# Optimization experiments

Hardware: AMD Instinct MI355X
Metric: run time of the kernel (lower is better)

Reference implementation:

```python
import jax, jax.numpy as jnp
import numpy as np

B, S, HID = 2, 4096, 2048
H, KV, D = 16, 4, 128
BS_, L, G, STRIDE, WTOK = 64, 4, 4, 4, 2048
SCALE = float(D) ** -0.5
NEG = -1.0e9


def _rope_tables(seq, dim):
    inv = 1.0 / (10000.0 ** (np.arange(0, dim, 2, dtype=np.float64) / dim))
    f = np.arange(seq, dtype=np.float64)[:, None] * inv[None, :]
    emb = np.concatenate([f, f], axis=-1)
    return np.cos(emb).astype(np.float32), np.sin(emb).astype(np.float32)


def _rotate_half(x):
    x1, x2 = x[..., : x.shape[-1] // 2], x[..., x.shape[-1] // 2 :]
    return jnp.concatenate([-x2, x1], axis=-1)


def _global_idx(nb, g, stride, max_away):
    # static (trace-time) computation of strided global block indices per query block
    g_idx = np.zeros((nb, g), dtype=np.int32)
    g_valid = np.zeros((nb, g), dtype=np.float32)
    for i in range(1, nb):
        cand = np.arange(max(0, i - max_away), i)
        if stride > 1:
            cand = cand[::stride]
        if cand.size == 0:
            continue
        if cand.size > g:
            cand = cand[-g:]
        s0 = g - cand.size
        g_idx[i, s0:] = cand
        g_valid[i, s0:] = 1.0
    return jnp.asarray(g_idx), jnp.asarray(g_valid)


def setup_inputs():
    key = jax.random.key(0)
    ks = jax.random.split(key, 5)
    hidden_states = jax.random.normal(ks[0], (B, S, HID), jnp.float32)
    cos_t, sin_t = _rope_tables(S, D)
    cos = jnp.broadcast_to(jnp.asarray(cos_t)[None], (B, S, D))
    sin = jnp.broadcast_to(jnp.asarray(sin_t)[None], (B, S, D))
    attention_mask_2d = jnp.ones((B, S), jnp.float32)
    sd = HID ** -0.5
    Wq = jax.random.normal(ks[1], (HID, H * D), jnp.float32) * sd
    Wk = jax.random.normal(ks[2], (HID, KV * D), jnp.float32) * sd
    Wv = jax.random.normal(ks[3], (HID, KV * D), jnp.float32) * sd
    Wo = jax.random.normal(ks[4], (H * D, HID), jnp.float32) * sd
    return dict(hidden_states=hidden_states, cos=cos, sin=sin,
                attention_mask_2d=attention_mask_2d, Wq=Wq, Wk=Wk, Wv=Wv, Wo=Wo)


def reference(hidden_states, cos, sin, attention_mask_2d, Wq, Wk, Wv, Wo):
    b, s, _ = hidden_states.shape
    q = (hidden_states @ Wq).reshape(b, s, H, D).transpose(0, 2, 1, 3)   # [b,H,s,d]
    k = (hidden_states @ Wk).reshape(b, s, KV, D).transpose(0, 2, 1, 3)  # [b,KV,s,d]
    v = (hidden_states @ Wv).reshape(b, s, KV, D).transpose(0, 2, 1, 3)
    c, sn = cos[:, None], sin[:, None]
    q = q * c + _rotate_half(q) * sn
    k = k * c + _rotate_half(k) * sn
    rep = H // KV
    k = jnp.repeat(k, rep, axis=1)
    v = jnp.repeat(v, rep, axis=1)

    nb = s // BS_
    qb = q.reshape(b, H, nb, BS_, D)
    kb = k.reshape(b, H, nb, BS_, D)
    vb = v.reshape(b, H, nb, BS_, D)
    km = attention_mask_2d.reshape(b, nb, BS_)

    # local window of L previous-or-current blocks (left-padded with zero blocks)
    pad = L - 1
    kp = jnp.pad(kb, ((0, 0), (0, 0), (pad, 0), (0, 0), (0, 0)))
    vp = jnp.pad(vb, ((0, 0), (0, 0), (pad, 0), (0, 0), (0, 0)))
    kmp = jnp.pad(km, ((0, 0), (pad, 0), (0, 0)))
    k_loc = jnp.stack([kp[:, :, w : w + nb] for w in range(L)], axis=3)   # [b,H,nb,L,BS,d]
    v_loc = jnp.stack([vp[:, :, w : w + nb] for w in range(L)], axis=3)
    km_loc = jnp.stack([kmp[:, w : w + nb] for w in range(L)], axis=2)    # [b,nb,L,BS]

    s_loc = jnp.einsum('bhqtd,bhqwsd->bhqtws', qb, k_loc) * SCALE
    s_loc = s_loc + (1.0 - km_loc)[:, None, :, None] * NEG
    ar = jnp.arange(BS_)
    intra = jnp.where(ar[None, :] > ar[:, None], NEG, 0.0)  # causal inside current block
    s_loc = s_loc.at[:, :, :, :, -1, :].add(intra)

    # strided global blocks
    g_idx, g_valid = _global_idx(nb, G, STRIDE, max(1, WTOK // BS_))
    k_g = kb[:, :, g_idx]   # [b,H,nb,G,BS,d]
    v_g = vb[:, :, g_idx]
    km_g = km[:, g_idx] * g_valid[None, :, :, None]  # [b,nb,G,BS]
    s_g = jnp.einsum('bhqtd,bhqwsd->bhqtws', qb, k_g) * SCALE
    s_g = s_g + (1.0 - km_g)[:, None, :, None] * NEG

    scores = jnp.concatenate([s_loc.reshape(b, H, nb, BS_, L * BS_),
                              s_g.reshape(b, H, nb, BS_, G * BS_)], axis=-1)
    v_all = jnp.concatenate([v_loc.reshape(b, H, nb, L * BS_, D),
                             v_g.reshape(b, H, nb, G * BS_, D)], axis=3)
    probs = jax.nn.softmax(scores, axis=-1)
    out = jnp.einsum('bhqtk,bhqkd->bhqtd', probs, v_all)
    out = out.reshape(b, H, s, D).transpose(0, 2, 1, 3).reshape(b, s, H * D)
    return out @ Wo
```

## Files before the change

kernel.cpp:

```cpp
#include <hip/hip_runtime.h>
#include <hip/hip_bf16.h>

typedef __hip_bfloat16 bf16;
typedef __attribute__((ext_vector_type(8))) short v8s;
typedef __attribute__((ext_vector_type(4))) short v4s;
typedef __attribute__((ext_vector_type(4))) float v4f;

#define MFMA(a, b, c) __builtin_amdgcn_mfma_f32_16x16x32_bf16((a), (b), (c), 0, 0, 0)

static constexpr int BB = 2, SEQ = 4096, HIDN = 2048, NH = 16, NKV = 4, HD = 128;
static constexpr float SCALE = 0.08838834764831845f;
static constexpr float NEGV = -1e9f;

__device__ __forceinline__ bf16 f2b(float x) { return __float2bfloat16(x); }

__device__ __forceinline__ void glds16(const bf16* g, bf16* l) {
  __builtin_amdgcn_global_load_lds(
      (const __attribute__((address_space(1))) unsigned int*)g,
      (__attribute__((address_space(3))) unsigned int*)l, 16, 0, 0);
}

__global__ void convert_k(const float* __restrict__ X, bf16* __restrict__ Y, long n) {
  long i4 = ((long)blockIdx.x * 256 + threadIdx.x) * 4;
  if (i4 >= n) return;
  v4f x = *(const v4f*)(X + i4);
  bf16 t[4];
#pragma unroll
  for (int j = 0; j < 4; j++) t[j] = f2b(x[j]);
  *(v4s*)(Y + i4) = *(const v4s*)t;
}

__global__ void transpose_k(const float* __restrict__ W, bf16* __restrict__ Wt,
                            int K, int N) {
  long idx = (long)blockIdx.x * 256 + threadIdx.x;
  if (idx >= (long)K * N) return;
  int k = (int)(idx % K);
  int n = (int)(idx / K);
  Wt[idx] = f2b(W[(long)k * N + n]);
}

template <int MODE, typename OT>
__global__ __launch_bounds__(256) void gemm128(const bf16* __restrict__ A,
                                               const bf16* __restrict__ Bt,
                                               OT* __restrict__ C,
                                               int M, int N, int K) {
  __shared__ __align__(16) bf16 As[2][128 * 32];
  __shared__ __align__(16) bf16 Bs[2][128 * 32];

  const int tid = threadIdx.x;
  const int lane = tid & 63, wv = tid >> 6;
  const int wr = wv >> 1, wc = wv & 1;
  const int l15 = lane & 15, quad = lane >> 4;
  const int m0 = blockIdx.y * 128, n0 = blockIdx.x * 128;

  const bf16* aSrc = A + (long)(m0 + (tid >> 2)) * K + (tid & 3) * 8;
  const bf16* bSrc = Bt + (long)(n0 + (tid >> 2)) * K + (tid & 3) * 8;
  const long rowStride = (long)64 * K;

  int aoff[4], boff[4];
#pragma unroll
  for (int t = 0; t < 4; t++) {
    aoff[t] = (wr * 64 + t * 16 + l15) * 32 + quad * 8;
    boff[t] = (wc * 64 + t * 16 + l15) * 32 + quad * 8;
  }

  v4f acc[4][4];
#pragma unroll
  for (int i = 0; i < 4; i++)
#pragma unroll
    for (int j = 0; j < 4; j++) acc[i][j] = {0.f, 0.f, 0.f, 0.f};

  const int nIter = K >> 5;
  for (int it = 0; it < nIter; ++it) {
    const int kc = it << 5;
    const int bsel = it & 1;
    bf16* aD = As[bsel] + wv * 512;
    bf16* bD = Bs[bsel] + wv * 512;
    glds16(aSrc + kc, aD);
    glds16(aSrc + rowStride + kc, aD + 2048);
    glds16(bSrc + kc, bD);
    glds16(bSrc + rowStride + kc, bD + 2048);
    asm volatile("s_waitcnt vmcnt(0)" ::: "memory");
    __syncthreads();

    const bf16* Ab = As[bsel];
    const bf16* Bb = Bs[bsel];
    v8s af[4], bfv[4];
#pragma unroll
    for (int t = 0; t < 4; t++) {
      af[t] = *(const v8s*)(Ab + aoff[t]);
      bfv[t] = *(const v8s*)(Bb + boff[t]);
    }
#pragma unroll
    for (int i = 0; i < 4; i++)
#pragma unroll
      for (int j = 0; j < 4; j++) acc[i][j] = MFMA(af[i], bfv[j], acc[i][j]);
  }

#pragma unroll
  for (int i = 0; i < 4; i++)
#pragma unroll
    for (int j = 0; j < 4; j++)
#pragma unroll
      for (int r = 0; r < 4; r++) {
        int m = m0 + wr * 64 + i * 16 + quad * 4 + r;
        int n = n0 + wc * 64 + j * 16 + l15;
        long addr;
        if (MODE == 0) {
          addr = (long)m * N + n;
        } else {
          int bb = m >> 12, s = m & (SEQ - 1);
          int hh = n >> 7, d = n & (HD - 1);
          if (MODE == 1)      addr = ((long)(bb * NH + hh) * SEQ + s) * HD + d;
          else if (MODE == 2) addr = ((long)(bb * NKV + hh) * SEQ + s) * HD + d;
          else                addr = ((long)(bb * NKV + hh) * HD + d) * SEQ + s;
        }
        float v = acc[i][j][r];
        if constexpr (sizeof(OT) == 2) C[addr] = f2b(v);
        else                           C[addr] = v;
      }
}

__global__ void rope_k(bf16* __restrict__ X, const float* __restrict__ cs,
                       const float* __restrict__ sn, int nheads) {
  int idx = blockIdx.x * 256 + threadIdx.x;
  int d = idx & 63;
  int row = idx >> 6;
  int s = row & (SEQ - 1);
  int bh = row >> 12;
  int b = bh / nheads;
  long xo = (long)row * HD;
  long co = ((long)b * SEQ + s) * HD;
  float x1 = __bfloat162float(X[xo + d]), x2 = __bfloat162float(X[xo + d + 64]);
  float c1 = cs[co + d], c2 = cs[co + d + 64];
  float s1 = sn[co + d], s2 = sn[co + d + 64];
  X[xo + d] = f2b(x1 * c1 - x2 * s1);
  X[xo + d + 64] = f2b(x2 * c2 + x1 * s2);
}

__global__ __launch_bounds__(256) void attn_k(const bf16* __restrict__ Q,
                                              const bf16* __restrict__ K,
                                              const bf16* __restrict__ V,
                                              const float* __restrict__ msk,
                                              bf16* __restrict__ ctx) {
  const int i = blockIdx.x >> 2, j = blockIdx.x & 3;
  const int kv = blockIdx.y, b = blockIdx.z;
  const int lane = threadIdx.x & 63, wv = threadIdx.x >> 6;
  const int h = kv * 4 + wv;
  const int l15 = lane & 15, quad = lane >> 4;

  __shared__ __align__(16) bf16 kvs[2][8192];
  __shared__ __align__(16) bf16 pb[4][16][72];

  int kb[8];
  bool kval[8];
#pragma unroll
  for (int w = 0; w < 4; w++) { kb[w] = i - 3 + w; kval[w] = (kb[w] >= 0); }
  {
    int st = i - 32; if (st < 0) st = 0;
    int n = i - st;
    int cnt = (n + 3) >> 2;
#pragma unroll
    for (int t = 0; t < 4; t++) {
      int jj = cnt + t - 4;
      kval[4 + t] = (jj >= 0);
      kb[4 + t] = (jj >= 0) ? (st + 4 * jj) : 0;
    }
  }
  int kbc[8];
#pragma unroll
  for (int t = 0; t < 8; t++) kbc[t] = kb[t] < 0 ? 0 : kb[t];

  const bf16* qp = Q + ((long)(b * NH + h) * SEQ + i * 64 + j * 16 + l15) * HD + quad * 8;
  v8s qf[4];
#pragma unroll
  for (int kk = 0; kk < 4; kk++) qf[kk] = *(const v8s*)(qp + kk * 32);

  const int klr = lane >> 4, kgp = lane & 15;
  const int vlr = lane >> 3, vgp = lane & 7;

  const bf16* gk = K + (long)(b * NKV + kv) * SEQ * HD;
  const bf16* gv = V + (long)(b * NKV + kv) * HD * SEQ;

  auto stageK = [&](int blk, bf16* dst) {
    const bf16* kbase = gk + (long)blk * 64 * HD;
#pragma unroll
    for (int c = 0; c < 4; c++) {
      int tl = wv * 16 + c * 4 + klr;
      int g = kgp ^ (tl & 15);
      glds16(kbase + (long)tl * HD + g * 8, dst + (wv * 16 + c * 4) * 128);
    }
  };
  auto stageV = [&](int blk, bf16* dst) {
    const bf16* vbase = gv + (long)blk * 64;
#pragma unroll
    for (int c = 0; c < 4; c++) {
      int row = wv * 32 + c * 8 + vlr;
      int g = vgp ^ (row & 7);
      glds16(vbase + (long)row * SEQ + g * 8, dst + (wv * 32 + c * 8) * 64);
    }
  };

  v4f sacc[32];
#pragma unroll
  for (int T = 0; T < 32; T++) sacc[T] = {0.f, 0.f, 0.f, 0.f};

  stageK(kbc[0], kvs[0]);
  asm volatile("s_waitcnt vmcnt(0)" ::: "memory");
  __syncthreads();

  for (int it = 0; it < 8; ++it) {
    const int bsel = it & 1;
    if (it < 7) stageK(kbc[it + 1], kvs[bsel ^ 1]);

    const bf16* Kb = kvs[bsel];
    __builtin_amdgcn_s_setprio(1);
#pragma unroll
    for (int t = 0; t < 4; t++) {
      v4f a = sacc[it * 4 + t];
#pragma unroll
      for (int kk = 0; kk < 4; kk++) {
        int off = (t * 16 + l15) * 128 + (((kk * 4 + quad) ^ l15) * 8);
        a = MFMA(qf[kk], *(const v8s*)(Kb + off), a);
      }
      sacc[it * 4 + t] = a;
    }
    __builtin_amdgcn_s_setprio(0);
    __syncthreads();
  }

  stageV(kbc[0], kvs[0]);

#pragma unroll
  for (int kbi = 0; kbi < 8; kbi++) {
    if (!kval[kbi]) {
#pragma unroll
      for (int t = 0; t < 4; t++) sacc[kbi * 4 + t] = {NEGV, NEGV, NEGV, NEGV};
      continue;
    }
#pragma unroll
    for (int t = 0; t < 4; t++) {
      int tok = kb[kbi] * 64 + t * 16 + l15;
      float madd = (1.0f - msk[b * SEQ + tok]) * NEGV;
      v4f sv = sacc[kbi * 4 + t];
#pragma unroll
      for (int r = 0; r < 4; r++) {
        float x = sv[r] * SCALE + madd;
        if (kbi == 3) {
          int kpp = t * 16 + l15;
          int qpp = j * 16 + quad * 4 + r;
          if (kpp > qpp) x += NEGV;
        }
        sv[r] = x;
      }
      sacc[kbi * 4 + t] = sv;
    }
  }

  float rmax[4] = {-3.4e38f, -3.4e38f, -3.4e38f, -3.4e38f};
#pragma unroll
  for (int T = 0; T < 32; T++)
#pragma unroll
    for (int r = 0; r < 4; r++) rmax[r] = fmaxf(rmax[r], sacc[T][r]);
#pragma unroll
  for (int m = 1; m <= 8; m <<= 1)
#pragma unroll
    for (int r = 0; r < 4; r++) rmax[r] = fmaxf(rmax[r], __shfl_xor(rmax[r], m, 64));

  float rsum[4] = {0.f, 0.f, 0.f, 0.f};
#pragma unroll
  for (int T = 0; T < 32; T++)
#pragma unroll
    for (int r = 0; r < 4; r++) {
      float e = __expf(sacc[T][r] - rmax[r]);
      sacc[T][r] = e;
      rsum[r] += e;
    }
#pragma unroll
  for (int m = 1; m <= 8; m <<= 1)
#pragma unroll
    for (int r = 0; r < 4; r++) rsum[r] += __shfl_xor(rsum[r], m, 64);

  v4f oacc[8] = {{0.f, 0.f, 0.f, 0.f}, {0.f, 0.f, 0.f, 0.f}, {0.f, 0.f, 0.f, 0.f},
                 {0.f, 0.f, 0.f, 0.f}, {0.f, 0.f, 0.f, 0.f}, {0.f, 0.f, 0.f, 0.f},
                 {0.f, 0.f, 0.f, 0.f}, {0.f, 0.f, 0.f, 0.f}};

  asm volatile("s_waitcnt vmcnt(0)" ::: "memory");
  __syncthreads();

  for (int it = 0; it < 8; ++it) {
    const int bsel = it & 1;
    if (it < 7) stageV(kbc[it + 1], kvs[bsel ^ 1]);

#pragma unroll
    for (int t = 0; t < 4; t++)
#pragma unroll
      for (int r = 0; r < 4; r++)
        pb[wv][quad * 4 + r][t * 16 + l15] = f2b(sacc[it * 4 + t][r]);

    const bf16* Vb = kvs[bsel];
    __builtin_amdgcn_s_setprio(1);
#pragma unroll
    for (int hf = 0; hf < 2; hf++) {
      v8s af = *(const v8s*)&pb[wv][l15][hf * 32 + quad * 8];
#pragma unroll
      for (int nt = 0; nt < 8; nt++) {
        int off = (nt * 16 + l15) * 64 + (((hf * 4 + quad) ^ (l15 & 7)) * 8);
        oacc[nt] = MFMA(af, *(const v8s*)(Vb + off), oacc[nt]);
      }
    }
    __builtin_amdgcn_s_setprio(0);
    __syncthreads();
  }

  const int tokw = i * 64 + j * 16 + quad * 4;
#pragma unroll
  for (int nt = 0; nt < 8; nt++)
#pragma unroll
    for (int r = 0; r < 4; r++) {
      float v = oacc[nt][r] / rsum[r];
      long addr = ((long)b * SEQ + tokw + r) * (NH * HD) + h * HD + nt * 16 + l15;
      ctx[addr] = f2b(v);
    }
}

extern "C" void kernel_launch(void* const* d_in, const int* in_sizes, int n_in,
                              void* d_out, int out_size, void* d_ws, size_t ws_size,
                              hipStream_t stream) {
  const float* hs  = (const float*)d_in[0];
  const float* cs  = (const float*)d_in[1];
  const float* sn  = (const float*)d_in[2];
  const float* msk = (const float*)d_in[3];
  const float* Wq  = (const float*)d_in[4];
  const float* Wk  = (const float*)d_in[5];
  const float* Wv  = (const float*)d_in[6];
  const float* Wo  = (const float*)d_in[7];
  float* out = (float*)d_out;

  char* w = (char*)d_ws;
  bf16* hsb = (bf16*)w; w += (size_t)BB * SEQ * HIDN * 2;
  bf16* Wqt = (bf16*)w; w += (size_t)2048 * 2048 * 2;
  bf16* Wkt = (bf16*)w; w += (size_t)512 * 2048 * 2;
  bf16* Wvt = (bf16*)w; w += (size_t)512 * 2048 * 2;
  bf16* Wot = (bf16*)w; w += (size_t)2048 * 2048 * 2;
  bf16* Qr  = (bf16*)w; w += (size_t)BB * NH * SEQ * HD * 2;
  bf16* Kr  = (bf16*)w; w += (size_t)BB * NKV * SEQ * HD * 2;
  bf16* Vt  = (bf16*)w; w += (size_t)BB * NKV * HD * SEQ * 2;
  bf16* ctx = hsb;

  long nhs = (long)BB * SEQ * HIDN;
  convert_k<<<(int)(nhs / 4 / 256), 256, 0, stream>>>(hs, hsb, nhs);

  transpose_k<<<(2048 * 2048) / 256, 256, 0, stream>>>(Wq, Wqt, 2048, 2048);
  transpose_k<<<(2048 * 512) / 256, 256, 0, stream>>>(Wk, Wkt, 2048, 512);
  transpose_k<<<(2048 * 512) / 256, 256, 0, stream>>>(Wv, Wvt, 2048, 512);
  transpose_k<<<(2048 * 2048) / 256, 256, 0, stream>>>(Wo, Wot, 2048, 2048);

  gemm128<1, bf16><<<dim3(2048 / 128, 8192 / 128), 256, 0, stream>>>(hsb, Wqt, Qr, 8192, 2048, 2048);
  gemm128<2, bf16><<<dim3(512 / 128, 8192 / 128), 256, 0, stream>>>(hsb, Wkt, Kr, 8192, 512, 2048);
  gemm128<3, bf16><<<dim3(512 / 128, 8192 / 128), 256, 0, stream>>>(hsb, Wvt, Vt, 8192, 512, 2048);

  rope_k<<<(BB * NH * SEQ * 64) / 256, 256, 0, stream>>>(Qr, cs, sn, NH);
  rope_k<<<(BB * NKV * SEQ * 64) / 256, 256, 0, stream>>>(Kr, cs, sn, NKV);

  attn_k<<<dim3(256, 4, 2), 256, 0, stream>>>(Qr, Kr, Vt, msk, ctx);

  gemm128<0, float><<<dim3(2048 / 128, 8192 / 128), 256, 0, stream>>>(ctx, Wot, out, 8192, 2048, 2048);
}
```

Before: 640.7 us.

## Recompute QK scores in two passes to cut registers; tile weight transpose via LDS

The attention kernel no longer keeps 32 fp32 score accumulators live. A first QK pass computes only the raw row max. A second pass recomputes the scores, applies the mask, exponentiates and stores the probabilities packed as bf16 pairs, and launch bounds now request 3 blocks per CU. This trades an extra QK MFMA pass and a second K staging for lower register pressure and higher occupancy. The weight transpose kernel also changes from a strided per-element gather to an LDS-tiled 64x64 transpose with coalesced reads and writes.

```diff
diff --git a/kernel.cpp b/kernel.cpp
--- a/kernel.cpp
+++ b/kernel.cpp
@@ -13,6 +13,12 @@
 static constexpr float NEGV = -1e9f;
 
 __device__ __forceinline__ bf16 f2b(float x) { return __float2bfloat16(x); }
+
+__device__ __forceinline__ unsigned int packbf2(float a, float b) {
+  union { bf16 h; unsigned short u; } ua, ub;
+  ua.h = f2b(a); ub.h = f2b(b);
+  return (unsigned int)ua.u | ((unsigned int)ub.u << 16);
+}
 
 __device__ __forceinline__ void glds16(const bf16* g, bf16* l) {
   __builtin_amdgcn_global_load_lds(
@@ -30,13 +36,19 @@
   *(v4s*)(Y + i4) = *(const v4s*)t;
 }
 
-__global__ void transpose_k(const float* __restrict__ W, bf16* __restrict__ Wt,
-                            int K, int N) {
-  long idx = (long)blockIdx.x * 256 + threadIdx.x;
-  if (idx >= (long)K * N) return;
-  int k = (int)(idx % K);
-  int n = (int)(idx / K);
-  Wt[idx] = f2b(W[(long)k * N + n]);
+__global__ __launch_bounds__(256) void transpose_k(const float* __restrict__ W,
+                                                   bf16* __restrict__ Wt,
+                                                   int K, int N) {
+  __shared__ bf16 tile[64][65];
+  const int tx = threadIdx.x & 63, ty = threadIdx.x >> 6;
+  const int k0 = blockIdx.y << 6, n0 = blockIdx.x << 6;
+#pragma unroll
+  for (int rr = 0; rr < 64; rr += 4)
+    tile[tx][rr + ty] = f2b(W[(long)(k0 + rr + ty) * N + n0 + tx]);
+  __syncthreads();
+#pragma unroll
+  for (int rr = 0; rr < 64; rr += 4)
+    Wt[(long)(n0 + rr + ty) * K + k0 + tx] = tile[rr + ty][tx];
 }
 
 template <int MODE, typename OT>
@@ -138,11 +150,11 @@
   X[xo + d + 64] = f2b(x2 * c2 + x1 * s2);
 }
 
-__global__ __launch_bounds__(256) void attn_k(const bf16* __restrict__ Q,
-                                              const bf16* __restrict__ K,
-                                              const bf16* __restrict__ V,
-                                              const float* __restrict__ msk,
-                                              bf16* __restrict__ ctx) {
+__global__ __launch_bounds__(256, 3) void attn_k(const bf16* __restrict__ Q,
+                                                 const bf16* __restrict__ K,
+                                                 const bf16* __restrict__ V,
+                                                 const float* __restrict__ msk,
+                                                 bf16* __restrict__ ctx) {
   const int i = blockIdx.x >> 2, j = blockIdx.x & 3;
   const int kv = blockIdx.y, b = blockIdx.z;
   const int lane = threadIdx.x & 63, wv = threadIdx.x >> 6;
@@ -150,7 +162,7 @@
   const int l15 = lane & 15, quad = lane >> 4;
 
   __shared__ __align__(16) bf16 kvs[2][8192];
-  __shared__ __align__(16) bf16 pb[4][16][72];
+  __shared__ __align__(16) unsigned short pb[4][16][72];
 
   int kb[8];
   bool kval[8];
@@ -201,9 +213,7 @@
     }
   };
 
-  v4f sacc[32];
-#pragma unroll
-  for (int T = 0; T < 32; T++) sacc[T] = {0.f, 0.f, 0.f, 0.f};
+  float rmax[4] = {-3.4e38f, -3.4e38f, -3.4e38f, -3.4e38f};
 
   stageK(kbc[0], kvs[0]);
   asm volatile("s_waitcnt vmcnt(0)" ::: "memory");
@@ -212,70 +222,73 @@
   for (int it = 0; it < 8; ++it) {
     const int bsel = it & 1;
     if (it < 7) stageK(kbc[it + 1], kvs[bsel ^ 1]);
-
     const bf16* Kb = kvs[bsel];
     __builtin_amdgcn_s_setprio(1);
 #pragma unroll
     for (int t = 0; t < 4; t++) {
-      v4f a = sacc[it * 4 + t];
+      v4f a = {0.f, 0.f, 0.f, 0.f};
 #pragma unroll
       for (int kk = 0; kk < 4; kk++) {
         int off = (t * 16 + l15) * 128 + (((kk * 4 + quad) ^ l15) * 8);
         a = MFMA(qf[kk], *(const v8s*)(Kb + off), a);
       }
-      sacc[it * 4 + t] = a;
+#pragma unroll
+      for (int r = 0; r < 4; r++) rmax[r] = fmaxf(rmax[r], a[r]);
     }
     __builtin_amdgcn_s_setprio(0);
     __syncthreads();
   }
 
-  stageV(kbc[0], kvs[0]);
-
-#pragma unroll
-  for (int kbi = 0; kbi < 8; kbi++) {
-    if (!kval[kbi]) {
-#pragma unroll
-      for (int t = 0; t < 4; t++) sacc[kbi * 4 + t] = {NEGV, NEGV, NEGV, NEGV};
-      continue;
-    }
+#pragma unroll
+  for (int m = 1; m <= 8; m <<= 1)
+#pragma unroll
+    for (int r = 0; r < 4; r++) rmax[r] = fmaxf(rmax[r], __shfl_xor(rmax[r], m, 64));
+  float mrow[4];
+#pragma unroll
+  for (int r = 0; r < 4; r++) mrow[r] = rmax[r] * SCALE;
+
+  unsigned int p16[8][8];
+  float rsum[4] = {0.f, 0.f, 0.f, 0.f};
+
+  stageK(kbc[0], kvs[0]);
+  asm volatile("s_waitcnt vmcnt(0)" ::: "memory");
+  __syncthreads();
+
+#pragma unroll
+  for (int it = 0; it < 8; ++it) {
+    const int bsel = it & 1;
+    if (it < 7) stageK(kbc[it + 1], kvs[bsel ^ 1]);
+    const bf16* Kb = kvs[bsel];
+    __builtin_amdgcn_s_setprio(1);
 #pragma unroll
     for (int t = 0; t < 4; t++) {
-      int tok = kb[kbi] * 64 + t * 16 + l15;
-      float madd = (1.0f - msk[b * SEQ + tok]) * NEGV;
-      v4f sv = sacc[kbi * 4 + t];
+      v4f a = {0.f, 0.f, 0.f, 0.f};
+#pragma unroll
+      for (int kk = 0; kk < 4; kk++) {
+        int off = (t * 16 + l15) * 128 + (((kk * 4 + quad) ^ l15) * 8);
+        a = MFMA(qf[kk], *(const v8s*)(Kb + off), a);
+      }
+      int tokc = kbc[it] * 64 + t * 16 + l15;
+      float madd = kval[it] ? (1.0f - msk[b * SEQ + tokc]) * NEGV : NEGV;
 #pragma unroll
       for (int r = 0; r < 4; r++) {
-        float x = sv[r] * SCALE + madd;
-        if (kbi == 3) {
+        float x = a[r] * SCALE + madd;
+        if (it == 3) {
           int kpp = t * 16 + l15;
           int qpp = j * 16 + quad * 4 + r;
           if (kpp > qpp) x += NEGV;
         }
-        sv[r] = x;
-      }
-      sacc[kbi * 4 + t] = sv;
-    }
-  }
-
-  float rmax[4] = {-3.4e38f, -3.4e38f, -3.4e38f, -3.4e38f};
-#pragma unroll
-  for (int T = 0; T < 32; T++)
-#pragma unroll
-    for (int r = 0; r < 4; r++) rmax[r] = fmaxf(rmax[r], sacc[T][r]);
-#pragma unroll
-  for (int m = 1; m <= 8; m <<= 1)
-#pragma unroll
-    for (int r = 0; r < 4; r++) rmax[r] = fmaxf(rmax[r], __shfl_xor(rmax[r], m, 64));
-
-  float rsum[4] = {0.f, 0.f, 0.f, 0.f};
-#pragma unroll
-  for (int T = 0; T < 32; T++)
-#pragma unroll
-    for (int r = 0; r < 4; r++) {
-      float e = __expf(sacc[T][r] - rmax[r]);
-      sacc[T][r] = e;
-      rsum[r] += e;
-    }
+        float e = __expf(x - mrow[r]);
+        rsum[r] += e;
+        a[r] = e;
+      }
+      p16[it][t * 2 + 0] = packbf2(a[0], a[1]);
+      p16[it][t * 2 + 1] = packbf2(a[2], a[3]);
+    }
+    __builtin_amdgcn_s_setprio(0);
+    __syncthreads();
+  }
+
 #pragma unroll
   for (int m = 1; m <= 8; m <<= 1)
 #pragma unroll
@@ -285,9 +298,11 @@
                  {0.f, 0.f, 0.f, 0.f}, {0.f, 0.f, 0.f, 0.f}, {0.f, 0.f, 0.f, 0.f},
                  {0.f, 0.f, 0.f, 0.f}, {0.f, 0.f, 0.f, 0.f}};
 
+  stageV(kbc[0], kvs[0]);
   asm volatile("s_waitcnt vmcnt(0)" ::: "memory");
   __syncthreads();
 
+#pragma unroll
   for (int it = 0; it < 8; ++it) {
     const int bsel = it & 1;
     if (it < 7) stageV(kbc[it + 1], kvs[bsel ^ 1]);
@@ -295,8 +310,12 @@
 #pragma unroll
     for (int t = 0; t < 4; t++)
 #pragma unroll
-      for (int r = 0; r < 4; r++)
-        pb[wv][quad * 4 + r][t * 16 + l15] = f2b(sacc[it * 4 + t][r]);
+      for (int r = 0; r < 4; r++) {
+        unsigned int pr = p16[it][t * 2 + (r >> 1)];
+        unsigned short u = (r & 1) ? (unsigned short)(pr >> 16)
+                                   : (unsigned short)(pr & 0xffff);
+        pb[wv][quad * 4 + r][t * 16 + l15] = u;
+      }
 
     const bf16* Vb = kvs[bsel];
     __builtin_amdgcn_s_setprio(1);
@@ -351,10 +370,10 @@
   long nhs = (long)BB * SEQ * HIDN;
   convert_k<<<(int)(nhs / 4 / 256), 256, 0, stream>>>(hs, hsb, nhs);
 
-  transpose_k<<<(2048 * 2048) / 256, 256, 0, stream>>>(Wq, Wqt, 2048, 2048);
-  transpose_k<<<(2048 * 512) / 256, 256, 0, stream>>>(Wk, Wkt, 2048, 512);
-  transpose_k<<<(2048 * 512) / 256, 256, 0, stream>>>(Wv, Wvt, 2048, 512);
-  transpose_k<<<(2048 * 2048) / 256, 256, 0, stream>>>(Wo, Wot, 2048, 2048);
+  transpose_k<<<dim3(2048 / 64, 2048 / 64), 256, 0, stream>>>(Wq, Wqt, 2048, 2048);
+  transpose_k<<<dim3(512 / 64, 2048 / 64), 256, 0, stream>>>(Wk, Wkt, 2048, 512);
+  transpose_k<<<dim3(512 / 64, 2048 / 64), 256, 0, stream>>>(Wv, Wvt, 2048, 512);
+  transpose_k<<<dim3(2048 / 64, 2048 / 64), 256, 0, stream>>>(Wo, Wot, 2048, 2048);
 
   gemm128<1, bf16><<<dim3(2048 / 128, 8192 / 128), 256, 0, stream>>>(hsb, Wqt, Qr, 8192, 2048, 2048);
   gemm128<2, bf16><<<dim3(512 / 128, 8192 / 128), 256, 0, stream>>>(hsb, Wkt, Kr, 8192, 512, 2048);
```

Result: faster. 606.0 us (-5.4%).
